# Kernel optimization log

Hardware: AMD Instinct MI355X
Metric: run time of the kernel (lower is better)

Reference implementation:

```python
import jax, jax.numpy as jnp
import numpy as np

LOW_DIM, SKIP_DIM, OUT_DIM = 512, 256, 256
EPS_IDW = 1e-8
EPS_LN = 1e-5
K = 3


def setup_inputs() -> dict:
    key = jax.random.key(0)
    ks = jax.random.split(key, 10)
    B, N, S = 4, 8192, 2048
    xyz_hi = jax.random.uniform(ks[0], (B, N, 3), dtype=jnp.float32)
    xyz_lo = jax.random.uniform(ks[1], (B, S, 3), dtype=jnp.float32)
    feat_skip = jax.random.normal(ks[2], (B, N, SKIP_DIM), dtype=jnp.float32)
    feat_lo = jax.random.normal(ks[3], (B, S, LOW_DIM), dtype=jnp.float32)
    in_dim = LOW_DIM + SKIP_DIM
    W1 = jax.random.normal(ks[4], (in_dim, OUT_DIM), dtype=jnp.float32) / np.sqrt(in_dim)
    b1 = jnp.zeros((OUT_DIM,), dtype=jnp.float32)
    W2 = jax.random.normal(ks[5], (OUT_DIM, OUT_DIM), dtype=jnp.float32) / np.sqrt(OUT_DIM)
    b2 = jnp.zeros((OUT_DIM,), dtype=jnp.float32)
    gamma = jnp.ones((OUT_DIM,), dtype=jnp.float32)
    beta = jnp.zeros((OUT_DIM,), dtype=jnp.float32)
    return {"xyz_hi": xyz_hi, "xyz_lo": xyz_lo, "feat_skip": feat_skip,
            "feat_lo": feat_lo, "W1": W1, "b1": b1, "W2": W2, "b2": b2,
            "gamma": gamma, "beta": beta}


def _layer_norm(x, gamma, beta):
    mu = jnp.mean(x, axis=-1, keepdims=True)
    var = jnp.mean(jnp.square(x - mu), axis=-1, keepdims=True)
    return (x - mu) * jax.lax.rsqrt(var + EPS_LN) * gamma + beta


def reference(xyz_hi, xyz_lo, feat_skip, feat_lo, W1, b1, W2, b2, gamma, beta):
    B, N, _ = xyz_hi.shape
    _, S, _ = xyz_lo.shape
    if S == 1:
        interpolated = jnp.broadcast_to(feat_lo, (B, N, feat_lo.shape[-1]))
    else:
        # pairwise Euclidean distances: (B, N, S)
        d2 = (jnp.sum(xyz_hi ** 2, -1)[:, :, None]
              + jnp.sum(xyz_lo ** 2, -1)[:, None, :]
              - 2.0 * jnp.einsum('bnd,bsd->bns', xyz_hi, xyz_lo))
        dists = jnp.sqrt(jnp.maximum(d2, 0.0))
        # smallest-3 via top_k on negated distances
        neg_d, knn_idx = jax.lax.top_k(-dists, K)          # (B, N, 3)
        dk = -neg_d
        inv_d = 1.0 / (dk + EPS_IDW)
        weights = inv_d / jnp.sum(inv_d, axis=-1, keepdims=True)  # (B, N, 3)
        # gather neighbor features: (B, N, 3, low_dim)
        knn_feat = feat_lo[jnp.arange(B)[:, None, None], knn_idx]
        interpolated = jnp.einsum('bnk,bnkc->bnc', weights, knn_feat)
    fused = jnp.concatenate([feat_skip, interpolated], axis=-1)   # (B, N, skip+low)
    h = jax.nn.relu(fused @ W1 + b1)
    h = h @ W2 + b2
    return _layer_norm(h, gamma, beta)
```

## Files before the change

### kernel.cpp

```cpp
#include <hip/hip_runtime.h>
#include <hip/hip_bf16.h>
#include <stdint.h>

typedef unsigned short u16;
typedef __attribute__((ext_vector_type(8))) short short8;
typedef __attribute__((ext_vector_type(4))) float f32x4;

#define BB 4
#define NN 8192
#define SS 2048
#define MTOT 32768
#define CSKIP 256
#define CLO 512
#define CIN 768
#define COUT 256

__device__ __forceinline__ u16 f2bf(float f) {
  unsigned u = __float_as_uint(f);
  u += 0x7fffu + ((u >> 16) & 1u);
  return (u16)(u >> 16);
}

__device__ __forceinline__ void gl_lds16(const void* g, void* l) {
  __builtin_amdgcn_global_load_lds(
      (const __attribute__((address_space(1))) void*)g,
      (__attribute__((address_space(3))) void*)l, 16, 0, 0);
}

__global__ __launch_bounds__(1024) void knn_wconv_kernel(
    const float* __restrict__ xyz_hi, const float* __restrict__ xyz_lo,
    const float* __restrict__ W1, const float* __restrict__ W2,
    float* __restrict__ wq_g, int* __restrict__ iq_g,
    u16* __restrict__ W1aT, u16* __restrict__ W1bT, u16* __restrict__ W2T) {
  int blk = blockIdx.x;
  int tid = threadIdx.x;
  if (blk >= 512) {
    int base = (blk - 512) * 1024 + tid;
    for (int i = base; i < 262144; i += 65536) {
      if (i < 65536) {
        int n = i >> 8, k = i & 255;
        W1aT[i] = f2bf(W1[(size_t)k * COUT + n]);
      } else if (i < 196608) {
        int j = i - 65536;
        int n = j >> 9, k = j & 511;
        W1bT[j] = f2bf(W1[(size_t)(256 + k) * COUT + n]);
      } else {
        int j = i - 196608;
        int n = j >> 8, k = j & 255;
        W2T[j] = f2bf(W2[(size_t)k * COUT + n]);
      }
    }
    return;
  }

  __shared__ float md[16][64][3];
  __shared__ int   mi[16][64][3];

  int b = blk >> 7;
  int wave = tid >> 6, lane = tid & 63;
  int qm = blk * 64 + lane;
  float qx = xyz_hi[(size_t)qm * 3 + 0];
  float qy = xyz_hi[(size_t)qm * 3 + 1];
  float qz = xyz_hi[(size_t)qm * 3 + 2];

  const float* xl = xyz_lo + (size_t)b * SS * 3;
  int j0 = __builtin_amdgcn_readfirstlane(wave * 128);

  float b0 = 1e30f, b1 = 1e30f, b2 = 1e30f;
  int i0 = -1, i1 = -1, i2 = -1;
#pragma unroll 8
  for (int jj = 0; jj < 128; ++jj) {
    int j = j0 + jj;
    float px = xl[3 * j + 0];
    float py = xl[3 * j + 1];
    float pz = xl[3 * j + 2];
    float dx = px - qx, dy = py - qy, dz = pz - qz;
    float d = fmaf(dx, dx, fmaf(dy, dy, dz * dz));
    bool c0 = d < b0, c1 = d < b1, c2 = d < b2;
    float nb0 = fminf(b0, d);
    float nb1 = __builtin_amdgcn_fmed3f(b0, b1, d);
    float nb2 = __builtin_amdgcn_fmed3f(b1, b2, d);
    int ni0 = c0 ? j : i0;
    int ni1 = c0 ? i0 : (c1 ? j : i1);
    int ni2 = c1 ? i1 : (c2 ? j : i2);
    b0 = nb0; b1 = nb1; b2 = nb2;
    i0 = ni0; i1 = ni1; i2 = ni2;
  }
  md[wave][lane][0] = b0; mi[wave][lane][0] = i0;
  md[wave][lane][1] = b1; mi[wave][lane][1] = i1;
  md[wave][lane][2] = b2; mi[wave][lane][2] = i2;
  __syncthreads();

  if (tid < 64) {
    int q = tid;
    float fb0 = 1e30f, fb1 = 1e30f, fb2 = 1e30f;
    int fi0 = -1, fi1 = -1, fi2 = -1;
    for (int p = 0; p < 16; ++p)
#pragma unroll
      for (int s = 0; s < 3; ++s) {
        float d = md[p][q][s]; int ix = mi[p][q][s];
        if (d < fb2 || (d == fb2 && ix < fi2)) {
          fb2 = d; fi2 = ix;
          if (fb2 < fb1 || (fb2 == fb1 && fi2 < fi1)) {
            float t = fb1; fb1 = fb2; fb2 = t; int ti = fi1; fi1 = fi2; fi2 = ti;
          }
          if (fb1 < fb0 || (fb1 == fb0 && fi1 < fi0)) {
            float t = fb0; fb0 = fb1; fb1 = t; int ti = fi0; fi0 = fi1; fi1 = ti;
          }
        }
      }
    int qm2 = blk * 64 + q;
    float d0 = sqrtf(fb0), d1 = sqrtf(fb1), d2 = sqrtf(fb2);
    float inv0 = 1.0f / (d0 + 1e-8f);
    float inv1 = 1.0f / (d1 + 1e-8f);
    float inv2 = 1.0f / (d2 + 1e-8f);
    float s = inv0 + inv1 + inv2;
    wq_g[(size_t)qm2 * 3 + 0] = inv0 / s;
    wq_g[(size_t)qm2 * 3 + 1] = inv1 / s;
    wq_g[(size_t)qm2 * 3 + 2] = inv2 / s;
    iq_g[(size_t)qm2 * 3 + 0] = fi0;
    iq_g[(size_t)qm2 * 3 + 1] = fi1;
    iq_g[(size_t)qm2 * 3 + 2] = fi2;
  }
}

__global__ __launch_bounds__(256, 4) void ggemm_kernel(
    const float* __restrict__ feat_lo, const u16* __restrict__ W1bT,
    float* __restrict__ G) {
  __shared__ u16 As[2][32 * 40];
  __shared__ u16 Bs[2][128 * 32];
  int tid = threadIdx.x;
  int m0 = (blockIdx.x >> 1) << 5;
  int n0 = (blockIdx.x & 1) << 7;
  int w = tid >> 6, lane = tid & 63;
  int quad = lane >> 4, l16 = lane & 15;

  int srow = tid >> 3, s4 = (tid & 7) << 2;
  const float* arow = feat_lo + (size_t)(m0 + srow) * CLO + s4;

  f32x4 zero = {0.f, 0.f, 0.f, 0.f};
  f32x4 acc[2][2];
#pragma unroll
  for (int tm = 0; tm < 2; ++tm)
#pragma unroll
    for (int tn = 0; tn < 2; ++tn) acc[tm][tn] = zero;

#pragma unroll
  for (int r = 0; r < 2; ++r) {
    int u = tid + r * 256;
    int nrow = u >> 2, c = u & 3;
    int cg = c ^ (nrow & 3);
    gl_lds16(W1bT + (size_t)(n0 + nrow) * CLO + cg * 8, (char*)Bs[0] + u * 16);
  }
  {
    float4 av = *(const float4*)(arow);
    union { __hip_bfloat162 h2[2]; uint2 u2; } pk;
    pk.h2[0] = __float22bfloat162_rn(make_float2(av.x, av.y));
    pk.h2[1] = __float22bfloat162_rn(make_float2(av.z, av.w));
    *(uint2*)(As[0] + srow * 40 + s4) = pk.u2;
  }

  for (int kc = 0; kc < 16; ++kc) {
    __syncthreads();
    const u16* Ac = As[kc & 1];
    const u16* Bc = Bs[kc & 1];
    if (kc + 1 < 16) {
      u16* An = As[(kc + 1) & 1];
      u16* Bn = Bs[(kc + 1) & 1];
#pragma unroll
      for (int r = 0; r < 2; ++r) {
        int u = tid + r * 256;
        int nrow = u >> 2, c = u & 3;
        int cg = c ^ (nrow & 3);
        gl_lds16(W1bT + (size_t)(n0 + nrow) * CLO + (kc + 1) * 32 + cg * 8,
                 (char*)Bn + u * 16);
      }
      float4 av = *(const float4*)(arow + (kc + 1) * 32);
      union { __hip_bfloat162 h2[2]; uint2 u2; } pk;
      pk.h2[0] = __float22bfloat162_rn(make_float2(av.x, av.y));
      pk.h2[1] = __float22bfloat162_rn(make_float2(av.z, av.w));
      *(uint2*)(An + srow * 40 + s4) = pk.u2;
    }

    short8 af[2], bf[2];
#pragma unroll
    for (int t = 0; t < 2; ++t)
      af[t] = *(const short8*)(Ac + (t * 16 + l16) * 40 + quad * 8);
#pragma unroll
    for (int t = 0; t < 2; ++t) {
      int rr = w * 32 + t * 16 + l16;
      bf[t] = *(const short8*)(Bc + (rr * 4 + (quad ^ (rr & 3))) * 8);
    }
#pragma unroll
    for (int tm = 0; tm < 2; ++tm)
#pragma unroll
      for (int tn = 0; tn < 2; ++tn)
        acc[tm][tn] = __builtin_amdgcn_mfma_f32_16x16x32_bf16(af[tm], bf[tn], acc[tm][tn], 0, 0, 0);
  }

#pragma unroll
  for (int tm = 0; tm < 2; ++tm)
#pragma unroll
    for (int tn = 0; tn < 2; ++tn) {
      int col = n0 + w * 32 + tn * 16 + l16;
#pragma unroll
      for (int r = 0; r < 4; ++r) {
        int row = m0 + tm * 16 + quad * 4 + r;
        G[(size_t)row * COUT + col] = acc[tm][tn][r];
      }
    }
}

__global__ __launch_bounds__(256, 2) void gemm12_kernel(
    const float* __restrict__ feat_skip, const u16* __restrict__ W1aT,
    const float* __restrict__ b1, const float* __restrict__ G,
    const float* __restrict__ wq_g, const int* __restrict__ iq_g,
    const u16* __restrict__ W2T, const float* __restrict__ b2,
    const float* __restrict__ gamma, const float* __restrict__ beta,
    float* __restrict__ out) {
  __shared__ u16 Hs[64 * 264];
  __shared__ u16 Bs[256 * 32];
  __shared__ u16 Bs2[256 * 32];
  __shared__ u16 As[2][64 * 40];
  __shared__ float swq[192];
  __shared__ int   siq[192];
  __shared__ float red[4][64][2];
  __shared__ float stats[64][2];
  int tid = threadIdx.x;
  int m0 = blockIdx.x << 6;
  int bS = (m0 >> 13) * SS;
  int w = tid >> 6, lane = tid & 63;
  int quad = lane >> 4, l16 = lane & 15;

  if (tid < 192) {
    swq[tid] = wq_g[(size_t)m0 * 3 + tid];
    siq[tid] = iq_g[(size_t)m0 * 3 + tid];
  }

  int srow = tid >> 2, sc8 = (tid & 3) << 3;
  const float* arow = feat_skip + (size_t)(m0 + srow) * CSKIP + sc8;

  f32x4 zero = {0.f, 0.f, 0.f, 0.f};
  f32x4 acc[4][4];
#pragma unroll
  for (int tm = 0; tm < 4; ++tm)
#pragma unroll
    for (int tn = 0; tn < 4; ++tn) acc[tm][tn] = zero;

#pragma unroll
  for (int r = 0; r < 4; ++r) {
    int u = tid + r * 256;
    int nrow = u >> 2, c = u & 3;
    int cg = c ^ (nrow & 3);
    gl_lds16(W1aT + (size_t)nrow * CSKIP + cg * 8, (char*)Bs + u * 16);
  }
  {
    float4 x0 = *(const float4*)(arow);
    float4 x1 = *(const float4*)(arow + 4);
    union { __hip_bfloat162 h2[4]; uint4 u4; } pk;
    pk.h2[0] = __float22bfloat162_rn(make_float2(x0.x, x0.y));
    pk.h2[1] = __float22bfloat162_rn(make_float2(x0.z, x0.w));
    pk.h2[2] = __float22bfloat162_rn(make_float2(x1.x, x1.y));
    pk.h2[3] = __float22bfloat162_rn(make_float2(x1.z, x1.w));
    *(uint4*)(As[0] + srow * 40 + sc8) = pk.u4;
  }

  for (int kc = 0; kc < 8; ++kc) {
    __syncthreads();
    const u16* Ac = As[kc & 1];
    u16* Bc = (kc & 1) ? Bs2 : Bs;
    if (kc + 1 < 8) {
      u16* An = As[(kc + 1) & 1];
      u16* Bn = (kc & 1) ? Bs : Bs2;
#pragma unroll
      for (int r = 0; r < 4; ++r) {
        int u = tid + r * 256;
        int nrow = u >> 2, c = u & 3;
        int cg = c ^ (nrow & 3);
        gl_lds16(W1aT + (size_t)nrow * CSKIP + (kc + 1) * 32 + cg * 8,
                 (char*)Bn + u * 16);
      }
      float4 x0 = *(const float4*)(arow + (kc + 1) * 32);
      float4 x1 = *(const float4*)(arow + (kc + 1) * 32 + 4);
      union { __hip_bfloat162 h2[4]; uint4 u4; } pk;
      pk.h2[0] = __float22bfloat162_rn(make_float2(x0.x, x0.y));
      pk.h2[1] = __float22bfloat162_rn(make_float2(x0.z, x0.w));
      pk.h2[2] = __float22bfloat162_rn(make_float2(x1.x, x1.y));
      pk.h2[3] = __float22bfloat162_rn(make_float2(x1.z, x1.w));
      *(uint4*)(An + srow * 40 + sc8) = pk.u4;
    }

    short8 af[4], bf[4];
#pragma unroll
    for (int t = 0; t < 4; ++t)
      af[t] = *(const short8*)(Ac + (t * 16 + l16) * 40 + quad * 8);
#pragma unroll
    for (int t = 0; t < 4; ++t) {
      int rr = w * 64 + t * 16 + l16;
      bf[t] = *(const short8*)(Bc + (rr * 4 + (quad ^ (rr & 3))) * 8);
    }
#pragma unroll
    for (int tm = 0; tm < 4; ++tm)
#pragma unroll
      for (int tn = 0; tn < 4; ++tn)
        acc[tm][tn] = __builtin_amdgcn_mfma_f32_16x16x32_bf16(af[tm], bf[tn], acc[tm][tn], 0, 0, 0);
  }

  {
    float bias[4];
#pragma unroll
    for (int tn = 0; tn < 4; ++tn) bias[tn] = b1[w * 64 + tn * 16 + l16];
#pragma unroll
    for (int tm = 0; tm < 4; ++tm)
#pragma unroll
      for (int r = 0; r < 4; ++r) {
        int rl = tm * 16 + quad * 4 + r;
        float w0 = swq[rl * 3 + 0], w1 = swq[rl * 3 + 1], w2 = swq[rl * 3 + 2];
        const float* g0 = G + (size_t)(bS + siq[rl * 3 + 0]) * COUT;
        const float* g1 = G + (size_t)(bS + siq[rl * 3 + 1]) * COUT;
        const float* g2 = G + (size_t)(bS + siq[rl * 3 + 2]) * COUT;
#pragma unroll
        for (int tn = 0; tn < 4; ++tn) {
          int col = w * 64 + tn * 16 + l16;
          float gv = fmaf(w0, g0[col], fmaf(w1, g1[col], w2 * g2[col]));
          float v = acc[tm][tn][r] + bias[tn] + gv;
          v = v > 0.f ? v : 0.f;
          Hs[rl * 264 + col] = f2bf(v);
        }
      }
  }

#pragma unroll
  for (int tm = 0; tm < 4; ++tm)
#pragma unroll
    for (int tn = 0; tn < 4; ++tn) acc[tm][tn] = zero;

  __syncthreads();
#pragma unroll
  for (int r = 0; r < 4; ++r) {
    int u = tid + r * 256;
    int nrow = u >> 2, c = u & 3;
    int cg = c ^ (nrow & 3);
    gl_lds16(W2T + (size_t)nrow * COUT + cg * 8, (char*)Bs + u * 16);
  }
  for (int kc = 0; kc < 8; ++kc) {
    __syncthreads();
    u16* cur = (kc & 1) ? Bs2 : Bs;
    u16* nxt = (kc & 1) ? Bs : Bs2;
    if (kc + 1 < 8) {
#pragma unroll
      for (int r = 0; r < 4; ++r) {
        int u = tid + r * 256;
        int nrow = u >> 2, c = u & 3;
        int cg = c ^ (nrow & 3);
        gl_lds16(W2T + (size_t)nrow * COUT + (kc + 1) * 32 + cg * 8,
                 (char*)nxt + u * 16);
      }
    }
    short8 af[4], bf[4];
#pragma unroll
    for (int t = 0; t < 4; ++t)
      af[t] = *(const short8*)(Hs + (t * 16 + l16) * 264 + kc * 32 + quad * 8);
#pragma unroll
    for (int t = 0; t < 4; ++t) {
      int rr = w * 64 + t * 16 + l16;
      bf[t] = *(const short8*)(cur + (rr * 4 + (quad ^ (rr & 3))) * 8);
    }
#pragma unroll
    for (int tm = 0; tm < 4; ++tm)
#pragma unroll
      for (int tn = 0; tn < 4; ++tn)
        acc[tm][tn] = __builtin_amdgcn_mfma_f32_16x16x32_bf16(af[tm], bf[tn], acc[tm][tn], 0, 0, 0);
  }

  float bias[4], g[4], be[4];
#pragma unroll
  for (int tn = 0; tn < 4; ++tn) {
    int col = w * 64 + tn * 16 + l16;
    bias[tn] = b2[col]; g[tn] = gamma[col]; be[tn] = beta[col];
  }
#pragma unroll
  for (int tm = 0; tm < 4; ++tm)
#pragma unroll
    for (int r = 0; r < 4; ++r) {
      float s = 0.f, sq = 0.f;
#pragma unroll
      for (int tn = 0; tn < 4; ++tn) {
        float v = acc[tm][tn][r] + bias[tn];
        acc[tm][tn][r] = v;
        s += v; sq += v * v;
      }
#pragma unroll
      for (int msk = 1; msk < 16; msk <<= 1) {
        s += __shfl_xor(s, msk);
        sq += __shfl_xor(sq, msk);
      }
      if (l16 == 0) {
        int rl = tm * 16 + quad * 4 + r;
        red[w][rl][0] = s;
        red[w][rl][1] = sq;
      }
    }
  __syncthreads();
  if (tid < 64) {
    float s = red[0][tid][0] + red[1][tid][0] + red[2][tid][0] + red[3][tid][0];
    float sq = red[0][tid][1] + red[1][tid][1] + red[2][tid][1] + red[3][tid][1];
    float mu = s * (1.f / 256.f);
    float var = sq * (1.f / 256.f) - mu * mu;
    stats[tid][0] = mu;
    stats[tid][1] = rsqrtf(var + 1e-5f);
  }
  __syncthreads();
#pragma unroll
  for (int tm = 0; tm < 4; ++tm)
#pragma unroll
    for (int r = 0; r < 4; ++r) {
      int rl = tm * 16 + quad * 4 + r;
      float mu = stats[rl][0], rstd = stats[rl][1];
#pragma unroll
      for (int tn = 0; tn < 4; ++tn) {
        int col = w * 64 + tn * 16 + l16;
        out[(size_t)(m0 + rl) * COUT + col] = (acc[tm][tn][r] - mu) * rstd * g[tn] + be[tn];
      }
    }
}

extern "C" void kernel_launch(void* const* d_in, const int* in_sizes, int n_in,
                              void* d_out, int out_size, void* d_ws, size_t ws_size,
                              hipStream_t stream) {
  const float* xyz_hi    = (const float*)d_in[0];
  const float* xyz_lo    = (const float*)d_in[1];
  const float* feat_skip = (const float*)d_in[2];
  const float* feat_lo   = (const float*)d_in[3];
  const float* W1        = (const float*)d_in[4];
  const float* b1        = (const float*)d_in[5];
  const float* W2        = (const float*)d_in[6];
  const float* b2        = (const float*)d_in[7];
  const float* gamma     = (const float*)d_in[8];
  const float* beta      = (const float*)d_in[9];
  float* out = (float*)d_out;

  char* ws = (char*)d_ws;
  u16*   W1aT  = (u16*)(ws + 16777216);
  u16*   W1bT  = (u16*)(ws + 16908288);
  u16*   W2T   = (u16*)(ws + 17170432);
  float* wq_g  = (float*)(ws + 17301504);
  int*   iq_g  = (int*)(ws + 17694720);
  float* G     = (float*)(ws + 18087936);

  knn_wconv_kernel<<<576, 1024, 0, stream>>>(xyz_hi, xyz_lo, W1, W2,
                                             wq_g, iq_g, W1aT, W1bT, W2T);
  ggemm_kernel<<<(BB * SS) / 32 * 2, 256, 0, stream>>>(feat_lo, W1bT, G);
  gemm12_kernel<<<MTOT / 64, 256, 0, stream>>>(feat_skip, W1aT, b1, G, wq_g, iq_g,
                                               W2T, b2, gamma, beta, out);
}
```

Baseline: 178.5 us.

## Merge KNN search and feat_lo GEMM into one heterogeneous kernel launch

```diff
diff --git a/kernel.cpp b/kernel.cpp
--- a/kernel.cpp
+++ b/kernel.cpp
@@ -27,25 +27,24 @@
       (__attribute__((address_space(3))) void*)l, 16, 0, 0);
 }
 
-__global__ __launch_bounds__(1024) void knn_wconv_kernel(
+__global__ __launch_bounds__(256, 4) void knn_ggemm_kernel(
     const float* __restrict__ xyz_hi, const float* __restrict__ xyz_lo,
-    const float* __restrict__ W1, const float* __restrict__ W2,
+    const float* __restrict__ feat_lo, const float* __restrict__ W1,
+    const float* __restrict__ W2,
     float* __restrict__ wq_g, int* __restrict__ iq_g,
-    u16* __restrict__ W1aT, u16* __restrict__ W1bT, u16* __restrict__ W2T) {
+    u16* __restrict__ W1aT, u16* __restrict__ W2T, float* __restrict__ G) {
+  __shared__ __align__(16) char smem[21504];
   int blk = blockIdx.x;
   int tid = threadIdx.x;
-  if (blk >= 512) {
-    int base = (blk - 512) * 1024 + tid;
-    for (int i = base; i < 262144; i += 65536) {
+
+  if (blk >= 1024) {
+    int base = (blk - 1024) * 256 + tid;
+    for (int i = base; i < 131072; i += 16384) {
       if (i < 65536) {
         int n = i >> 8, k = i & 255;
         W1aT[i] = f2bf(W1[(size_t)k * COUT + n]);
-      } else if (i < 196608) {
+      } else {
         int j = i - 65536;
-        int n = j >> 9, k = j & 511;
-        W1bT[j] = f2bf(W1[(size_t)(256 + k) * COUT + n]);
-      } else {
-        int j = i - 196608;
         int n = j >> 8, k = j & 255;
         W2T[j] = f2bf(W2[(size_t)k * COUT + n]);
       }
@@ -53,8 +52,98 @@
     return;
   }
 
-  __shared__ float md[16][64][3];
-  __shared__ int   mi[16][64][3];
+  if (blk >= 512) {
+    u16* As0 = (u16*)smem;
+    u16* As1 = (u16*)(smem + 2560);
+    u16* Bs0 = (u16*)(smem + 5120);
+    u16* Bs1 = (u16*)(smem + 13312);
+    int bb = blk - 512;
+    int m0 = (bb >> 1) << 5;
+    int n0 = (bb & 1) << 7;
+    int w = tid >> 6, lane = tid & 63;
+    int quad = lane >> 4, l16 = lane & 15;
+
+    int srow = tid >> 3, s4 = (tid & 7) << 2;
+    const float* arow = feat_lo + (size_t)(m0 + srow) * CLO + s4;
+
+    int kk = tid >> 3;
+    int nb = (tid & 7) << 4;
+    int kq = kk >> 3, k7 = kk & 7;
+    const float* wrow = W1 + (size_t)(256 + kk) * COUT + n0 + nb;
+
+    f32x4 zero = {0.f, 0.f, 0.f, 0.f};
+    f32x4 acc[2][2];
+#pragma unroll
+    for (int tm = 0; tm < 2; ++tm)
+#pragma unroll
+      for (int tn = 0; tn < 2; ++tn) acc[tm][tn] = zero;
+
+    auto stageB = [&](u16* Bn, int kc) {
+      const float* src = wrow + (size_t)kc * (32 * COUT);
+#pragma unroll
+      for (int r = 0; r < 4; ++r) {
+        float4 v = *(const float4*)(src + r * 4);
+        int n = nb + r * 4;
+        Bn[(n + 0) * 32 + ((kq ^ 0) * 8) + k7] = f2bf(v.x);
+        Bn[(n + 1) * 32 + ((kq ^ 1) * 8) + k7] = f2bf(v.y);
+        Bn[(n + 2) * 32 + ((kq ^ 2) * 8) + k7] = f2bf(v.z);
+        Bn[(n + 3) * 32 + ((kq ^ 3) * 8) + k7] = f2bf(v.w);
+      }
+    };
+    auto stageA = [&](u16* An, int kc) {
+      float4 av = *(const float4*)(arow + kc * 32);
+      union { __hip_bfloat162 h2[2]; uint2 u2; } pk;
+      pk.h2[0] = __float22bfloat162_rn(make_float2(av.x, av.y));
+      pk.h2[1] = __float22bfloat162_rn(make_float2(av.z, av.w));
+      *(uint2*)(An + srow * 40 + s4) = pk.u2;
+    };
+
+    stageB(Bs0, 0);
+    stageA(As0, 0);
+
+    for (int kc = 0; kc < 16; ++kc) {
+      __syncthreads();
+      const u16* Ac = (kc & 1) ? As1 : As0;
+      const u16* Bc = (kc & 1) ? Bs1 : Bs0;
+      if (kc + 1 < 16) {
+        u16* An = (kc & 1) ? As0 : As1;
+        u16* Bn = (kc & 1) ? Bs0 : Bs1;
+        stageB(Bn, kc + 1);
+        stageA(An, kc + 1);
+      }
+
+      short8 af[2], bf[2];
+#pragma unroll
+      for (int t = 0; t < 2; ++t)
+        af[t] = *(const short8*)(Ac + (t * 16 + l16) * 40 + quad * 8);
+#pragma unroll
+      for (int t = 0; t < 2; ++t) {
+        int rr = w * 32 + t * 16 + l16;
+        bf[t] = *(const short8*)(Bc + (rr * 4 + (quad ^ (rr & 3))) * 8);
+      }
+#pragma unroll
+      for (int tm = 0; tm < 2; ++tm)
+#pragma unroll
+        for (int tn = 0; tn < 2; ++tn)
+          acc[tm][tn] = __builtin_amdgcn_mfma_f32_16x16x32_bf16(af[tm], bf[tn], acc[tm][tn], 0, 0, 0);
+    }
+
+#pragma unroll
+    for (int tm = 0; tm < 2; ++tm)
+#pragma unroll
+      for (int tn = 0; tn < 2; ++tn) {
+        int col = n0 + w * 32 + tn * 16 + l16;
+#pragma unroll
+        for (int r = 0; r < 4; ++r) {
+          int row = m0 + tm * 16 + quad * 4 + r;
+          G[(size_t)row * COUT + col] = acc[tm][tn][r];
+        }
+      }
+    return;
+  }
+
+  float (*md)[64][3] = (float(*)[64][3])smem;
+  int   (*mi)[64][3] = (int(*)[64][3])(smem + 3072);
 
   int b = blk >> 7;
   int wave = tid >> 6, lane = tid & 63;
@@ -64,12 +153,12 @@
   float qz = xyz_hi[(size_t)qm * 3 + 2];
 
   const float* xl = xyz_lo + (size_t)b * SS * 3;
-  int j0 = __builtin_amdgcn_readfirstlane(wave * 128);
+  int j0 = __builtin_amdgcn_readfirstlane(wave * 512);
 
   float b0 = 1e30f, b1 = 1e30f, b2 = 1e30f;
   int i0 = -1, i1 = -1, i2 = -1;
 #pragma unroll 8
-  for (int jj = 0; jj < 128; ++jj) {
+  for (int jj = 0; jj < 512; ++jj) {
     int j = j0 + jj;
     float px = xl[3 * j + 0];
     float py = xl[3 * j + 1];
@@ -95,7 +184,7 @@
     int q = tid;
     float fb0 = 1e30f, fb1 = 1e30f, fb2 = 1e30f;
     int fi0 = -1, fi1 = -1, fi2 = -1;
-    for (int p = 0; p < 16; ++p)
+    for (int p = 0; p < 4; ++p)
 #pragma unroll
       for (int s = 0; s < 3; ++s) {
         float d = md[p][q][s]; int ix = mi[p][q][s];
@@ -122,93 +211,6 @@
     iq_g[(size_t)qm2 * 3 + 1] = fi1;
     iq_g[(size_t)qm2 * 3 + 2] = fi2;
   }
-}
-
-__global__ __launch_bounds__(256, 4) void ggemm_kernel(
-    const float* __restrict__ feat_lo, const u16* __restrict__ W1bT,
-    float* __restrict__ G) {
-  __shared__ u16 As[2][32 * 40];
-  __shared__ u16 Bs[2][128 * 32];
-  int tid = threadIdx.x;
-  int m0 = (blockIdx.x >> 1) << 5;
-  int n0 = (blockIdx.x & 1) << 7;
-  int w = tid >> 6, lane = tid & 63;
-  int quad = lane >> 4, l16 = lane & 15;
-
-  int srow = tid >> 3, s4 = (tid & 7) << 2;
-  const float* arow = feat_lo + (size_t)(m0 + srow) * CLO + s4;
-
-  f32x4 zero = {0.f, 0.f, 0.f, 0.f};
-  f32x4 acc[2][2];
-#pragma unroll
-  for (int tm = 0; tm < 2; ++tm)
-#pragma unroll
-    for (int tn = 0; tn < 2; ++tn) acc[tm][tn] = zero;
-
-#pragma unroll
-  for (int r = 0; r < 2; ++r) {
-    int u = tid + r * 256;
-    int nrow = u >> 2, c = u & 3;
-    int cg = c ^ (nrow & 3);
-    gl_lds16(W1bT + (size_t)(n0 + nrow) * CLO + cg * 8, (char*)Bs[0] + u * 16);
-  }
-  {
-    float4 av = *(const float4*)(arow);
-    union { __hip_bfloat162 h2[2]; uint2 u2; } pk;
-    pk.h2[0] = __float22bfloat162_rn(make_float2(av.x, av.y));
-    pk.h2[1] = __float22bfloat162_rn(make_float2(av.z, av.w));
-    *(uint2*)(As[0] + srow * 40 + s4) = pk.u2;
-  }
-
-  for (int kc = 0; kc < 16; ++kc) {
-    __syncthreads();
-    const u16* Ac = As[kc & 1];
-    const u16* Bc = Bs[kc & 1];
-    if (kc + 1 < 16) {
-      u16* An = As[(kc + 1) & 1];
-      u16* Bn = Bs[(kc + 1) & 1];
-#pragma unroll
-      for (int r = 0; r < 2; ++r) {
-        int u = tid + r * 256;
-        int nrow = u >> 2, c = u & 3;
-        int cg = c ^ (nrow & 3);
-        gl_lds16(W1bT + (size_t)(n0 + nrow) * CLO + (kc + 1) * 32 + cg * 8,
-                 (char*)Bn + u * 16);
-      }
-      float4 av = *(const float4*)(arow + (kc + 1) * 32);
-      union { __hip_bfloat162 h2[2]; uint2 u2; } pk;
-      pk.h2[0] = __float22bfloat162_rn(make_float2(av.x, av.y));
-      pk.h2[1] = __float22bfloat162_rn(make_float2(av.z, av.w));
-      *(uint2*)(An + srow * 40 + s4) = pk.u2;
-    }
-
-    short8 af[2], bf[2];
-#pragma unroll
-    for (int t = 0; t < 2; ++t)
-      af[t] = *(const short8*)(Ac + (t * 16 + l16) * 40 + quad * 8);
-#pragma unroll
-    for (int t = 0; t < 2; ++t) {
-      int rr = w * 32 + t * 16 + l16;
-      bf[t] = *(const short8*)(Bc + (rr * 4 + (quad ^ (rr & 3))) * 8);
-    }
-#pragma unroll
-    for (int tm = 0; tm < 2; ++tm)
-#pragma unroll
-      for (int tn = 0; tn < 2; ++tn)
-        acc[tm][tn] = __builtin_amdgcn_mfma_f32_16x16x32_bf16(af[tm], bf[tn], acc[tm][tn], 0, 0, 0);
-  }
-
-#pragma unroll
-  for (int tm = 0; tm < 2; ++tm)
-#pragma unroll
-    for (int tn = 0; tn < 2; ++tn) {
-      int col = n0 + w * 32 + tn * 16 + l16;
-#pragma unroll
-      for (int r = 0; r < 4; ++r) {
-        int row = m0 + tm * 16 + quad * 4 + r;
-        G[(size_t)row * COUT + col] = acc[tm][tn][r];
-      }
-    }
 }
 
 __global__ __launch_bounds__(256, 2) void gemm12_kernel(
@@ -442,15 +444,13 @@
 
   char* ws = (char*)d_ws;
   u16*   W1aT  = (u16*)(ws + 16777216);
-  u16*   W1bT  = (u16*)(ws + 16908288);
   u16*   W2T   = (u16*)(ws + 17170432);
   float* wq_g  = (float*)(ws + 17301504);
   int*   iq_g  = (int*)(ws + 17694720);
   float* G     = (float*)(ws + 18087936);
 
-  knn_wconv_kernel<<<576, 1024, 0, stream>>>(xyz_hi, xyz_lo, W1, W2,
-                                             wq_g, iq_g, W1aT, W1bT, W2T);
-  ggemm_kernel<<<(BB * SS) / 32 * 2, 256, 0, stream>>>(feat_lo, W1bT, G);
+  knn_ggemm_kernel<<<1088, 256, 0, stream>>>(xyz_hi, xyz_lo, feat_lo, W1, W2,
+                                             wq_g, iq_g, W1aT, W2T, G);
   gemm12_kernel<<<MTOT / 64, 256, 0, stream>>>(feat_skip, W1aT, b1, G, wq_g, iq_g,
                                                W2T, b2, gamma, beta, out);
 }
```

New measurement: 187.4 us. +5.0%, slower.

## Pre-convert activations to swizzled bf16 inside the KNN kernel and DMA-load tiles

Applied to the files above, without the earlier changes.

```diff
diff --git a/kernel.cpp b/kernel.cpp
--- a/kernel.cpp
+++ b/kernel.cpp
@@ -27,16 +27,38 @@
       (__attribute__((address_space(3))) void*)l, 16, 0, 0);
 }
 
+__device__ __forceinline__ void conv_chunk(const float* s, u16* d) {
+  union { u16 a[8]; short8 v; } pk;
+#pragma unroll
+  for (int i = 0; i < 8; ++i) pk.a[i] = f2bf(s[i]);
+  *(short8*)d = pk.v;
+}
+
 __global__ __launch_bounds__(1024) void knn_wconv_kernel(
     const float* __restrict__ xyz_hi, const float* __restrict__ xyz_lo,
     const float* __restrict__ W1, const float* __restrict__ W2,
+    const float* __restrict__ feat_skip, const float* __restrict__ feat_lo,
     float* __restrict__ wq_g, int* __restrict__ iq_g,
-    u16* __restrict__ W1aT, u16* __restrict__ W1bT, u16* __restrict__ W2T) {
+    u16* __restrict__ W1aT, u16* __restrict__ W1bT, u16* __restrict__ W2T,
+    u16* __restrict__ FSB, u16* __restrict__ FLB) {
   int blk = blockIdx.x;
   int tid = threadIdx.x;
-  if (blk >= 512) {
-    int base = (blk - 512) * 1024 + tid;
-    for (int i = base; i < 262144; i += 65536) {
+
+  if ((blk % 5) == 4) {
+    int wtid = (blk / 5) * 1024 + tid;
+    for (int t = wtid; t < 1048576; t += 131072) {
+      int p = t & 3, r = (t >> 2) & 32767, kc = t >> 17;
+      int c = p ^ (r & 3);
+      conv_chunk(feat_skip + (size_t)r * CSKIP + kc * 32 + c * 8,
+                 FSB + (size_t)t * 8);
+    }
+    for (int t = wtid; t < 524288; t += 131072) {
+      int p = t & 3, r = (t >> 2) & 8191, kc = t >> 15;
+      int c = p ^ (r & 3);
+      conv_chunk(feat_lo + (size_t)r * CLO + kc * 32 + c * 8,
+                 FLB + (size_t)t * 8);
+    }
+    for (int i = wtid; i < 262144; i += 131072) {
       if (i < 65536) {
         int n = i >> 8, k = i & 255;
         W1aT[i] = f2bf(W1[(size_t)k * COUT + n]);
@@ -56,9 +78,10 @@
   __shared__ float md[16][64][3];
   __shared__ int   mi[16][64][3];
 
-  int b = blk >> 7;
+  int kblk = (blk / 5) * 4 + (blk % 5);
+  int b = kblk >> 7;
   int wave = tid >> 6, lane = tid & 63;
-  int qm = blk * 64 + lane;
+  int qm = kblk * 64 + lane;
   float qx = xyz_hi[(size_t)qm * 3 + 0];
   float qy = xyz_hi[(size_t)qm * 3 + 1];
   float qz = xyz_hi[(size_t)qm * 3 + 2];
@@ -109,7 +132,7 @@
           }
         }
       }
-    int qm2 = blk * 64 + q;
+    int qm2 = kblk * 64 + q;
     float d0 = sqrtf(fb0), d1 = sqrtf(fb1), d2 = sqrtf(fb2);
     float inv0 = 1.0f / (d0 + 1e-8f);
     float inv1 = 1.0f / (d1 + 1e-8f);
@@ -125,9 +148,9 @@
 }
 
 __global__ __launch_bounds__(256, 4) void ggemm_kernel(
-    const float* __restrict__ feat_lo, const u16* __restrict__ W1bT,
+    const u16* __restrict__ FLB, const u16* __restrict__ W1bT,
     float* __restrict__ G) {
-  __shared__ u16 As[2][32 * 40];
+  __shared__ u16 As[2][32 * 32];
   __shared__ u16 Bs[2][128 * 32];
   int tid = threadIdx.x;
   int m0 = (blockIdx.x >> 1) << 5;
@@ -135,9 +158,6 @@
   int w = tid >> 6, lane = tid & 63;
   int quad = lane >> 4, l16 = lane & 15;
 
-  int srow = tid >> 3, s4 = (tid & 7) << 2;
-  const float* arow = feat_lo + (size_t)(m0 + srow) * CLO + s4;
-
   f32x4 zero = {0.f, 0.f, 0.f, 0.f};
   f32x4 acc[2][2];
 #pragma unroll
@@ -145,47 +165,40 @@
 #pragma unroll
     for (int tn = 0; tn < 2; ++tn) acc[tm][tn] = zero;
 
-#pragma unroll
-  for (int r = 0; r < 2; ++r) {
-    int u = tid + r * 256;
-    int nrow = u >> 2, c = u & 3;
-    int cg = c ^ (nrow & 3);
-    gl_lds16(W1bT + (size_t)(n0 + nrow) * CLO + cg * 8, (char*)Bs[0] + u * 16);
-  }
-  {
-    float4 av = *(const float4*)(arow);
-    union { __hip_bfloat162 h2[2]; uint2 u2; } pk;
-    pk.h2[0] = __float22bfloat162_rn(make_float2(av.x, av.y));
-    pk.h2[1] = __float22bfloat162_rn(make_float2(av.z, av.w));
-    *(uint2*)(As[0] + srow * 40 + s4) = pk.u2;
-  }
+  auto stageA = [&](u16* An, int kc) {
+    if (tid < 128)
+      gl_lds16((const char*)(FLB + ((size_t)kc * NN + m0) * 32) + tid * 16,
+               (char*)An + tid * 16);
+  };
+  auto stageB = [&](u16* Bn, int kc) {
+#pragma unroll
+    for (int r = 0; r < 2; ++r) {
+      int u = tid + r * 256;
+      int nrow = u >> 2, c = u & 3;
+      int cg = c ^ (nrow & 3);
+      gl_lds16(W1bT + (size_t)(n0 + nrow) * CLO + kc * 32 + cg * 8,
+               (char*)Bn + u * 16);
+    }
+  };
+
+  stageB(Bs[0], 0);
+  stageA(As[0], 0);
 
   for (int kc = 0; kc < 16; ++kc) {
     __syncthreads();
     const u16* Ac = As[kc & 1];
     const u16* Bc = Bs[kc & 1];
     if (kc + 1 < 16) {
-      u16* An = As[(kc + 1) & 1];
-      u16* Bn = Bs[(kc + 1) & 1];
-#pragma unroll
-      for (int r = 0; r < 2; ++r) {
-        int u = tid + r * 256;
-        int nrow = u >> 2, c = u & 3;
-        int cg = c ^ (nrow & 3);
-        gl_lds16(W1bT + (size_t)(n0 + nrow) * CLO + (kc + 1) * 32 + cg * 8,
-                 (char*)Bn + u * 16);
-      }
-      float4 av = *(const float4*)(arow + (kc + 1) * 32);
-      union { __hip_bfloat162 h2[2]; uint2 u2; } pk;
-      pk.h2[0] = __float22bfloat162_rn(make_float2(av.x, av.y));
-      pk.h2[1] = __float22bfloat162_rn(make_float2(av.z, av.w));
-      *(uint2*)(An + srow * 40 + s4) = pk.u2;
+      stageB(Bs[(kc + 1) & 1], kc + 1);
+      stageA(As[(kc + 1) & 1], kc + 1);
     }
 
     short8 af[2], bf[2];
 #pragma unroll
-    for (int t = 0; t < 2; ++t)
-      af[t] = *(const short8*)(Ac + (t * 16 + l16) * 40 + quad * 8);
+    for (int t = 0; t < 2; ++t) {
+      int rr = t * 16 + l16;
+      af[t] = *(const short8*)(Ac + (rr * 4 + (quad ^ (rr & 3))) * 8);
+    }
 #pragma unroll
     for (int t = 0; t < 2; ++t) {
       int rr = w * 32 + t * 16 + l16;
@@ -212,7 +225,7 @@
 }
 
 __global__ __launch_bounds__(256, 2) void gemm12_kernel(
-    const float* __restrict__ feat_skip, const u16* __restrict__ W1aT,
+    const u16* __restrict__ FSB, const u16* __restrict__ W1aT,
     const float* __restrict__ b1, const float* __restrict__ G,
     const float* __restrict__ wq_g, const int* __restrict__ iq_g,
     const u16* __restrict__ W2T, const float* __restrict__ b2,
@@ -221,7 +234,7 @@
   __shared__ u16 Hs[64 * 264];
   __shared__ u16 Bs[256 * 32];
   __shared__ u16 Bs2[256 * 32];
-  __shared__ u16 As[2][64 * 40];
+  __shared__ u16 As[2][64 * 32];
   __shared__ float swq[192];
   __shared__ int   siq[192];
   __shared__ float red[4][64][2];
@@ -237,15 +250,17 @@
     siq[tid] = iq_g[(size_t)m0 * 3 + tid];
   }
 
-  int srow = tid >> 2, sc8 = (tid & 3) << 3;
-  const float* arow = feat_skip + (size_t)(m0 + srow) * CSKIP + sc8;
-
   f32x4 zero = {0.f, 0.f, 0.f, 0.f};
   f32x4 acc[4][4];
 #pragma unroll
   for (int tm = 0; tm < 4; ++tm)
 #pragma unroll
     for (int tn = 0; tn < 4; ++tn) acc[tm][tn] = zero;
+
+  auto stageA = [&](u16* An, int kc) {
+    gl_lds16((const char*)(FSB + ((size_t)kc * MTOT + m0) * 32) + tid * 16,
+             (char*)An + tid * 16);
+  };
 
 #pragma unroll
   for (int r = 0; r < 4; ++r) {
@@ -254,23 +269,13 @@
     int cg = c ^ (nrow & 3);
     gl_lds16(W1aT + (size_t)nrow * CSKIP + cg * 8, (char*)Bs + u * 16);
   }
-  {
-    float4 x0 = *(const float4*)(arow);
-    float4 x1 = *(const float4*)(arow + 4);
-    union { __hip_bfloat162 h2[4]; uint4 u4; } pk;
-    pk.h2[0] = __float22bfloat162_rn(make_float2(x0.x, x0.y));
-    pk.h2[1] = __float22bfloat162_rn(make_float2(x0.z, x0.w));
-    pk.h2[2] = __float22bfloat162_rn(make_float2(x1.x, x1.y));
-    pk.h2[3] = __float22bfloat162_rn(make_float2(x1.z, x1.w));
-    *(uint4*)(As[0] + srow * 40 + sc8) = pk.u4;
-  }
+  stageA(As[0], 0);
 
   for (int kc = 0; kc < 8; ++kc) {
     __syncthreads();
     const u16* Ac = As[kc & 1];
     u16* Bc = (kc & 1) ? Bs2 : Bs;
     if (kc + 1 < 8) {
-      u16* An = As[(kc + 1) & 1];
       u16* Bn = (kc & 1) ? Bs : Bs2;
 #pragma unroll
       for (int r = 0; r < 4; ++r) {
@@ -280,20 +285,15 @@
         gl_lds16(W1aT + (size_t)nrow * CSKIP + (kc + 1) * 32 + cg * 8,
                  (char*)Bn + u * 16);
       }
-      float4 x0 = *(const float4*)(arow + (kc + 1) * 32);
-      float4 x1 = *(const float4*)(arow + (kc + 1) * 32 + 4);
-      union { __hip_bfloat162 h2[4]; uint4 u4; } pk;
-      pk.h2[0] = __float22bfloat162_rn(make_float2(x0.x, x0.y));
-      pk.h2[1] = __float22bfloat162_rn(make_float2(x0.z, x0.w));
-      pk.h2[2] = __float22bfloat162_rn(make_float2(x1.x, x1.y));
-      pk.h2[3] = __float22bfloat162_rn(make_float2(x1.z, x1.w));
-      *(uint4*)(An + srow * 40 + sc8) = pk.u4;
+      stageA(As[(kc + 1) & 1], kc + 1);
     }
 
     short8 af[4], bf[4];
 #pragma unroll
-    for (int t = 0; t < 4; ++t)
-      af[t] = *(const short8*)(Ac + (t * 16 + l16) * 40 + quad * 8);
+    for (int t = 0; t < 4; ++t) {
+      int rr = t * 16 + l16;
+      af[t] = *(const short8*)(Ac + (rr * 4 + (quad ^ (rr & 3))) * 8);
+    }
 #pragma unroll
     for (int t = 0; t < 4; ++t) {
       int rr = w * 64 + t * 16 + l16;
@@ -441,16 +441,20 @@
   float* out = (float*)d_out;
 
   char* ws = (char*)d_ws;
+  u16*   FSB   = (u16*)(ws + 0);
   u16*   W1aT  = (u16*)(ws + 16777216);
   u16*   W1bT  = (u16*)(ws + 16908288);
   u16*   W2T   = (u16*)(ws + 17170432);
   float* wq_g  = (float*)(ws + 17301504);
   int*   iq_g  = (int*)(ws + 17694720);
   float* G     = (float*)(ws + 18087936);
-
-  knn_wconv_kernel<<<576, 1024, 0, stream>>>(xyz_hi, xyz_lo, W1, W2,
-                                             wq_g, iq_g, W1aT, W1bT, W2T);
-  ggemm_kernel<<<(BB * SS) / 32 * 2, 256, 0, stream>>>(feat_lo, W1bT, G);
-  gemm12_kernel<<<MTOT / 64, 256, 0, stream>>>(feat_skip, W1aT, b1, G, wq_g, iq_g,
+  u16*   FLB   = (u16*)(ws + 26476544);
+
+  knn_wconv_kernel<<<640, 1024, 0, stream>>>(xyz_hi, xyz_lo, W1, W2,
+                                             feat_skip, feat_lo,
+                                             wq_g, iq_g, W1aT, W1bT, W2T,
+                                             FSB, FLB);
+  ggemm_kernel<<<(BB * SS) / 32 * 2, 256, 0, stream>>>(FLB, W1bT, G);
+  gemm12_kernel<<<MTOT / 64, 256, 0, stream>>>(FSB, W1aT, b1, G, wq_g, iq_g,
                                                W2T, b2, gamma, beta, out);
 }
```

New measurement: 182.4 us. +2.2%, slower.
